# Kernel optimization log

Hardware: AMD Instinct MI355X
Metric: run time of the kernel (lower is better)

## Reference

```python
import jax, jax.numpy as jnp
import numpy as np

D_MODEL = 512
D_INNER = 1024   # expand * d_model
D_STATE = 16
DT_RANK = 32     # ceil(d_model / 16)
D_CONV = 4
BATCH = 4
SEQLEN = 2304
DILATIONS = (1, 2, 4)


def _dw(x, w, pad, dil=1):
    # depthwise 1D conv: x (B,C,L), w (C,1,K)
    return jax.lax.conv_general_dilated(
        x, w, window_strides=(1,), padding=[pad], rhs_dilation=(dil,),
        dimension_numbers=('NCH', 'OIH', 'NCH'), feature_group_count=x.shape[1])


def setup_inputs() -> dict:
    key = jax.random.key(0)
    ks = iter(jax.random.split(key, 32))
    nrm = lambda shape, s=0.02: jax.random.normal(next(ks), shape, jnp.float32) * s
    std = DT_RANK ** -0.5
    return dict(
        hidden_states=jax.random.normal(next(ks), (BATCH, SEQLEN, D_MODEL), jnp.float32),
        in_proj_w=nrm((5 * D_INNER, D_MODEL)),
        conv1d_w=nrm((D_INNER, 1, D_CONV), 0.2),
        conv1d_b=jnp.zeros((D_INNER,), jnp.float32),
        x_proj_w=nrm((DT_RANK + 2 * D_STATE, D_INNER)),
        dt_proj_w=jax.random.uniform(next(ks), (D_INNER, DT_RANK), jnp.float32, -std, std),
        dt_proj_b=jax.random.uniform(next(ks), (D_INNER,), jnp.float32, -5.0, -1.0),
        A_log=jnp.log(jnp.broadcast_to(jnp.arange(1, D_STATE + 1, dtype=jnp.float32), (D_INNER, D_STATE))),
        D=jnp.ones((D_INNER,), jnp.float32),
        out_proj_w=nrm((D_MODEL, 3 * D_INNER)),
        cb_local_w=nrm((D_MODEL, 1, 3), 0.2), cb_local_b=jnp.zeros((D_MODEL,), jnp.float32),
        cb_global_w=nrm((D_MODEL, 1, 1), 0.2), cb_global_b=jnp.zeros((D_MODEL,), jnp.float32),
        cb_pre_w=nrm((3, D_MODEL, 1, 1), 0.2), cb_pre_b=jnp.zeros((3, D_MODEL), jnp.float32),
        cb_dil_w=nrm((3, D_MODEL, 1, 3), 0.2), cb_dil_b=jnp.zeros((3, D_MODEL), jnp.float32),
        cb_ln_g=jnp.ones((4 * D_MODEL,), jnp.float32), cb_ln_b=jnp.zeros((4 * D_MODEL,), jnp.float32),
        cb_fuse_w=nrm((2 * D_MODEL, 4 * D_MODEL, 1)), cb_fuse_b=jnp.zeros((2 * D_MODEL,), jnp.float32),
    )


def reference(hidden_states, in_proj_w, conv1d_w, conv1d_b, x_proj_w, dt_proj_w,
              dt_proj_b, A_log, D, out_proj_w, cb_local_w, cb_local_b,
              cb_global_w, cb_global_b, cb_pre_w, cb_pre_b, cb_dil_w, cb_dil_b,
              cb_ln_g, cb_ln_b, cb_fuse_w, cb_fuse_b):
    B, L, dm = hidden_states.shape
    d_inner = D.shape[0]
    d_state = A_log.shape[1]
    dt_rank = dt_proj_w.shape[1]

    # in_proj -> (B, 5*d_inner, L)
    xz = jnp.einsum('ed,bld->bel', in_proj_w, hidden_states)
    xz_f = xz[:, :2 * d_inner]
    xz_b = xz[:, 2 * d_inner:4 * d_inner]
    xz_1 = xz[:, 4 * d_inner:]
    # bidirectional: stack forward and time-flipped backward along batch
    xzc = jnp.concatenate([xz_f, jnp.flip(xz_b, -1)], axis=0)  # (2B, 2*d_inner, L)
    x, z = xzc[:, :d_inner], xzc[:, d_inner:]

    # causal depthwise conv + SiLU
    kc = conv1d_w.shape[-1]
    x = _dw(x, conv1d_w, (kc - 1, 0)) + conv1d_b[None, :, None]
    x = jax.nn.silu(x)

    # x_proj -> dt, B, C
    x_dbl = jnp.einsum('kd,bdl->bkl', x_proj_w, x)
    dt = x_dbl[:, :dt_rank]
    Bm = x_dbl[:, dt_rank:dt_rank + d_state]
    Cm = x_dbl[:, dt_rank + d_state:]
    delta = jax.nn.softplus(jnp.einsum('dr,brl->bdl', dt_proj_w, dt) + dt_proj_b[None, :, None])
    A = -jnp.exp(A_log)  # (d, n)

    # selective scan over time
    delta_l = jnp.moveaxis(delta, 2, 0)  # (L, 2B, d)
    u_l = jnp.moveaxis(x, 2, 0)          # (L, 2B, d)
    B_l = jnp.moveaxis(Bm, 2, 0)         # (L, 2B, n)
    C_l = jnp.moveaxis(Cm, 2, 0)         # (L, 2B, n)

    def step(h, t):
        dl, ul, Bl, Cl = t
        dA = jnp.exp(dl[..., None] * A)                    # (2B, d, n)
        h = dA * h + (dl * ul)[..., None] * Bl[:, None, :]
        y = jnp.einsum('bdn,bn->bd', h, Cl)
        return h, y

    h0 = jnp.zeros((x.shape[0], d_inner, d_state), x.dtype)
    _, ys = jax.lax.scan(step, h0, (delta_l, u_l, B_l, C_l))
    y = jnp.moveaxis(ys, 0, 2)  # (2B, d, L)
    y = y + D[None, :, None] * x
    y = y * jax.nn.silu(z)
    out = jnp.concatenate([y[:B], jnp.flip(y[B:], -1)], axis=1)  # (B, 2*d_inner, L)

    # ConvBranch on xz_1 (2*dm channels -> split into xa, xc of dm each)
    xa, xc = xz_1[:, :dm], xz_1[:, dm:]
    local = jax.nn.gelu(_dw(xc, cb_local_w, (1, 1)) + cb_local_b[None, :, None], approximate=False)
    phi = jax.nn.relu(cb_global_w[:, 0, 0][None, :] * xc.mean(-1) + cb_global_b[None, :])  # (B, dm)
    feats = []
    for i, d in enumerate(DILATIONS):
        xp = cb_pre_w[i, :, 0, 0][None, :, None] * xa + cb_pre_b[i][None, :, None]
        feats.append(_dw(xp, cb_dil_w[i], (d, d), dil=d) + cb_dil_b[i][None, :, None])
    cat = jnp.concatenate(feats + [phi[:, :, None] * local], axis=1)  # (B, 4*dm, L)
    c = cat.transpose(0, 2, 1)
    mu = c.mean(-1, keepdims=True)
    var = c.var(-1, keepdims=True)
    c = (c - mu) / jnp.sqrt(var + 1e-5) * cb_ln_g + cb_ln_b
    cat = c.transpose(0, 2, 1)
    out_c = jnp.einsum('oc,bcl->bol', cb_fuse_w[:, :, 0], cat) + cb_fuse_b[None, :, None]  # (B, 2*d_inner... = d_inner? no: 2*dm, L)

    out_f = jnp.concatenate([out, out_c], axis=1)  # (B, 3*d_inner, L)
    return jnp.einsum('md,bdl->blm', out_proj_w, out_f)  # (B, L, d_model)
```

## Files before the change

kernel.cpp:

```cpp
#include <hip/hip_runtime.h>
#include <math.h>

#define L 2304
#define NB 4
#define NCH 36
#define STILE 64
#define SPAD 68
#define DLU_PAD 130

typedef __attribute__((ext_vector_type(8))) short short8v;
typedef __attribute__((ext_vector_type(4))) float f32x4;

__device__ inline unsigned short f2bf(float x) {
    unsigned u = __float_as_uint(x);
    return (unsigned short)((u + 0x7fffu + ((u >> 16) & 1u)) >> 16);
}
__device__ inline void split1(float x, unsigned short& h, unsigned short& l) {
    h = f2bf(x);
    float hf = __uint_as_float((unsigned)h << 16);
    l = f2bf(x - hf);
}

__device__ __forceinline__ void gload16(const unsigned short* g, unsigned short* l)
{
    __builtin_amdgcn_global_load_lds(
        (const __attribute__((address_space(1))) unsigned int*)g,
        (__attribute__((address_space(3))) unsigned int*)l, 16, 0, 0);
}

__device__ inline float row_reduce16(float v) {
    v += __int_as_float(__builtin_amdgcn_update_dpp(0, __float_as_int(v), 0xB1, 0xF, 0xF, true));
    v += __int_as_float(__builtin_amdgcn_update_dpp(0, __float_as_int(v), 0x4E, 0xF, 0xF, true));
    v += __int_as_float(__builtin_amdgcn_update_dpp(0, __float_as_int(v), 0x124, 0xF, 0xF, true));
    v += __int_as_float(__builtin_amdgcn_update_dpp(0, __float_as_int(v), 0x128, 0xF, 0xF, true));
    return v;
}

__global__ __launch_bounds__(256) void split_kernel(
    const float* __restrict__ src, unsigned short* __restrict__ hi,
    unsigned short* __restrict__ lo, int n)
{
    int i = (blockIdx.x * 256 + threadIdx.x) * 4;
    if (i >= n) return;
    float4 v = *(const float4*)(src + i);
    unsigned short h0, h1, h2, h3, l0, l1, l2, l3;
    split1(v.x, h0, l0); split1(v.y, h1, l1);
    split1(v.z, h2, l2); split1(v.w, h3, l3);
    ushort4 hv; hv.x = h0; hv.y = h1; hv.z = h2; hv.w = h3;
    ushort4 lv; lv.x = l0; lv.y = l1; lv.z = l2; lv.w = l3;
    *(ushort4*)(hi + i) = hv;
    *(ushort4*)(lo + i) = lv;
}

__global__ __launch_bounds__(256) void split_t_kernel(
    const float* __restrict__ src, unsigned short* __restrict__ hiT,
    unsigned short* __restrict__ loT, int C)
{
    __shared__ float tile[64][65];
    const int l0 = blockIdx.x * 64, c0 = blockIdx.y * 64;
    const int li = threadIdx.x & 63, q = threadIdx.x >> 6;
    for (int cc = q; cc < 64; cc += 4)
        tile[cc][li] = src[(long)(c0 + cc) * L + l0 + li];
    __syncthreads();
    const int ci = threadIdx.x & 63;
    for (int ll = q; ll < 64; ll += 4) {
        float x = tile[ci][ll];
        unsigned short h, l;
        split1(x, h, l);
        long o = (long)(l0 + ll) * C + c0 + ci;
        hiT[o] = h;
        loT[o] = l;
    }
}

__global__ __launch_bounds__(256) void gemm_mfma(
    const unsigned short* __restrict__ Ahi, const unsigned short* __restrict__ Alo, int lda,
    const unsigned short* __restrict__ Bhi, const unsigned short* __restrict__ Blo, int ldb,
    float* __restrict__ C, long cms, long cns, int K, int act,
    const float* __restrict__ emu, const float* __restrict__ ers,
    const float* __restrict__ es1, const float* __restrict__ es2)
{
    __shared__ unsigned short Ah[128 * 32], Al[128 * 32], Bh[128 * 32], Bl[128 * 32];
    const int tid = threadIdx.x;
    const int lane = tid & 63, wave = tid >> 6;
    const int wm = (wave >> 1) * 64, wn = (wave & 1) * 64;
    const int m0 = blockIdx.x * 128, n0 = blockIdx.y * 128;
    const int rowS = tid >> 2;
    const int cS = ((tid & 3) ^ ((tid >> 3) & 3)) * 8;
    const unsigned short* gAh0 = Ahi + (long)(m0 + rowS) * lda + cS;
    const unsigned short* gAl0 = Alo + (long)(m0 + rowS) * lda + cS;
    const unsigned short* gBh0 = Bhi + (long)(n0 + rowS) * ldb + cS;
    const unsigned short* gBl0 = Blo + (long)(n0 + rowS) * ldb + cS;
    const long a64 = (long)64 * lda, b64 = (long)64 * ldb;
    unsigned short* lAh0 = Ah + tid * 8;  unsigned short* lAh1 = Ah + 2048 + tid * 8;
    unsigned short* lAl0 = Al + tid * 8;  unsigned short* lAl1 = Al + 2048 + tid * 8;
    unsigned short* lBh0 = Bh + tid * 8;  unsigned short* lBh1 = Bh + 2048 + tid * 8;
    unsigned short* lBl0 = Bl + tid * 8;  unsigned short* lBl1 = Bl + 2048 + tid * 8;
    const int fr = lane & 15;
    const int chq = (((lane >> 4) ^ ((fr >> 1) & 3)) << 3);

    f32x4 acc[4][4];
#pragma unroll
    for (int i = 0; i < 4; ++i)
#pragma unroll
        for (int j = 0; j < 4; ++j) acc[i][j] = (f32x4){0.f, 0.f, 0.f, 0.f};

    for (int k0 = 0; k0 < K; k0 += 32) {
        gload16(gAh0 + k0, lAh0); gload16(gAh0 + a64 + k0, lAh1);
        gload16(gAl0 + k0, lAl0); gload16(gAl0 + a64 + k0, lAl1);
        gload16(gBh0 + k0, lBh0); gload16(gBh0 + b64 + k0, lBh1);
        gload16(gBl0 + k0, lBl0); gload16(gBl0 + b64 + k0, lBl1);
        __syncthreads();
        short8v bhf[4], blf[4];
#pragma unroll
        for (int nf = 0; nf < 4; ++nf) {
            bhf[nf] = *(const short8v*)&Bh[(wn + nf * 16 + fr) * 32 + chq];
            blf[nf] = *(const short8v*)&Bl[(wn + nf * 16 + fr) * 32 + chq];
        }
#pragma unroll
        for (int mf = 0; mf < 4; ++mf) {
            short8v ah = *(const short8v*)&Ah[(wm + mf * 16 + fr) * 32 + chq];
            short8v al = *(const short8v*)&Al[(wm + mf * 16 + fr) * 32 + chq];
#pragma unroll
            for (int nf = 0; nf < 4; ++nf) {
                acc[mf][nf] = __builtin_amdgcn_mfma_f32_16x16x32_bf16(ah, bhf[nf], acc[mf][nf], 0, 0, 0);
                acc[mf][nf] = __builtin_amdgcn_mfma_f32_16x16x32_bf16(ah, blf[nf], acc[mf][nf], 0, 0, 0);
                acc[mf][nf] = __builtin_amdgcn_mfma_f32_16x16x32_bf16(al, bhf[nf], acc[mf][nf], 0, 0, 0);
            }
        }
        __syncthreads();
    }
    const int rb = (lane >> 4) * 4;
#pragma unroll
    for (int mf = 0; mf < 4; ++mf) {
#pragma unroll
        for (int nf = 0; nf < 4; ++nf) {
            int n = n0 + wn + nf * 16 + fr;
            int mb = m0 + wm + mf * 16 + rb;
            if (cms == 1) {
                float4 r;
                r.x = acc[mf][nf][0]; r.y = acc[mf][nf][1];
                r.z = acc[mf][nf][2]; r.w = acc[mf][nf][3];
                *(float4*)(C + (long)n * cns + mb) = r;
            } else {
#pragma unroll
                for (int r = 0; r < 4; ++r) {
                    int m = mb + r;
                    float v = acc[mf][nf][r];
                    if (act == 2) v = (v - emu[n] * es1[m]) * ers[n] + es2[m];
                    C[(long)m * cms + n] = v;
                }
            }
        }
    }
}

__global__ __launch_bounds__(256) void gemm_mfma128sk(
    const unsigned short* __restrict__ Ahi, const unsigned short* __restrict__ Alo, int lda,
    const unsigned short* __restrict__ Bhi, const unsigned short* __restrict__ Blo, int ldb,
    float* __restrict__ P, int KS, int Mstride)
{
    __shared__ unsigned short Ah[128 * 32], Al[128 * 32], Bh[128 * 32], Bl[128 * 32];
    const int tid = threadIdx.x;
    const int lane = tid & 63, wave = tid >> 6;
    const int wm = (wave >> 1) * 64, wn = (wave & 1) * 64;
    const int nwg = gridDim.x * gridDim.y * gridDim.z;
    const int bid = blockIdx.x + gridDim.x * (blockIdx.y + gridDim.y * blockIdx.z);
    const int cpx = nwg >> 3;
    const int swz = (bid & 7) * cpx + (bid >> 3);
    const int bx = swz % gridDim.x;
    const int rest = swz / gridDim.x;
    const int by = rest % gridDim.y;
    const int sl = rest / gridDim.y;
    const int m0 = bx * 128, n0 = by * 128;
    const int kbase = sl * KS;
    const int rowS = tid >> 2;
    const int cS = ((tid & 3) ^ ((tid >> 3) & 3)) * 8;
    const unsigned short* gAh0 = Ahi + (long)(m0 + rowS) * lda + kbase + cS;
    const unsigned short* gAl0 = Alo + (long)(m0 + rowS) * lda + kbase + cS;
    const unsigned short* gBh0 = Bhi + (long)(n0 + rowS) * ldb + kbase + cS;
    const unsigned short* gBl0 = Blo + (long)(n0 + rowS) * ldb + kbase + cS;
    const long a64 = (long)64 * lda, b64 = (long)64 * ldb;
    unsigned short* lAh0 = Ah + tid * 8;  unsigned short* lAh1 = Ah + 2048 + tid * 8;
    unsigned short* lAl0 = Al + tid * 8;  unsigned short* lAl1 = Al + 2048 + tid * 8;
    unsigned short* lBh0 = Bh + tid * 8;  unsigned short* lBh1 = Bh + 2048 + tid * 8;
    unsigned short* lBl0 = Bl + tid * 8;  unsigned short* lBl1 = Bl + 2048 + tid * 8;
    const int fr = lane & 15;
    const int chq = (((lane >> 4) ^ ((fr >> 1) & 3)) << 3);

    f32x4 acc[4][4];
#pragma unroll
    for (int i = 0; i < 4; ++i)
#pragma unroll
        for (int j = 0; j < 4; ++j) acc[i][j] = (f32x4){0.f, 0.f, 0.f, 0.f};

    for (int k0 = 0; k0 < KS; k0 += 32) {
        gload16(gAh0 + k0, lAh0); gload16(gAh0 + a64 + k0, lAh1);
        gload16(gAl0 + k0, lAl0); gload16(gAl0 + a64 + k0, lAl1);
        gload16(gBh0 + k0, lBh0); gload16(gBh0 + b64 + k0, lBh1);
        gload16(gBl0 + k0, lBl0); gload16(gBl0 + b64 + k0, lBl1);
        __syncthreads();
        short8v bhf[4], blf[4];
#pragma unroll
        for (int nf = 0; nf < 4; ++nf) {
            bhf[nf] = *(const short8v*)&Bh[(wn + nf * 16 + fr) * 32 + chq];
            blf[nf] = *(const short8v*)&Bl[(wn + nf * 16 + fr) * 32 + chq];
        }
#pragma unroll
        for (int mf = 0; mf < 4; ++mf) {
            short8v ah = *(const short8v*)&Ah[(wm + mf * 16 + fr) * 32 + chq];
            short8v al = *(const short8v*)&Al[(wm + mf * 16 + fr) * 32 + chq];
#pragma unroll
            for (int nf = 0; nf < 4; ++nf) {
                acc[mf][nf] = __builtin_amdgcn_mfma_f32_16x16x32_bf16(ah, bhf[nf], acc[mf][nf], 0, 0, 0);
                acc[mf][nf] = __builtin_amdgcn_mfma_f32_16x16x32_bf16(ah, blf[nf], acc[mf][nf], 0, 0, 0);
                acc[mf][nf] = __builtin_amdgcn_mfma_f32_16x16x32_bf16(al, bhf[nf], acc[mf][nf], 0, 0, 0);
            }
        }
        __syncthreads();
    }
    const int rb = (lane >> 4) * 4;
    float* Pp = P + (long)sl * Mstride * L;
#pragma unroll
    for (int mf = 0; mf < 4; ++mf) {
#pragma unroll
        for (int nf = 0; nf < 4; ++nf) {
            int n = n0 + wn + nf * 16 + fr;
            int mb = m0 + wm + mf * 16 + rb;
            float4 r;
            r.x = acc[mf][nf][0]; r.y = acc[mf][nf][1];
            r.z = acc[mf][nf][2]; r.w = acc[mf][nf][3];
            *(float4*)(Pp + (long)n * Mstride + mb) = r;
        }
    }
}

__global__ __launch_bounds__(256) void out_reduce(
    const float* __restrict__ P, float* __restrict__ out)
{
    const long E = (long)512 * L;
    long i = ((long)blockIdx.x * 256 + threadIdx.x) * 4;
    float4 r = *(const float4*)(P + i);
#pragma unroll
    for (int s = 1; s < 8; ++s) {
        float4 a = *(const float4*)(P + (long)s * E + i);
        r.x += a.x; r.y += a.y; r.z += a.z; r.w += a.w;
    }
    *(float4*)(out + i) = r;
}

__global__ __launch_bounds__(256) void fuse_reduce_bt(
    const float* __restrict__ P,
    const float* __restrict__ emu, const float* __restrict__ ers,
    const float* __restrict__ es1, const float* __restrict__ es2,
    unsigned short* __restrict__ BT_hi, unsigned short* __restrict__ BT_lo)
{
    const long E = (long)1024 * L;
    long idx = (long)blockIdx.x * 256 + threadIdx.x;
    int l = (int)(idx >> 8);
    int dq = (int)(idx & 255) * 4;
    long base = (long)l * 1024 + dq;
    float4 a = *(const float4*)(P + base);
    float4 b = *(const float4*)(P + E + base);
    float4 c = *(const float4*)(P + 2 * E + base);
    float4 d = *(const float4*)(P + 3 * E + base);
    float v[4];
    v[0] = (a.x + b.x) + (c.x + d.x);
    v[1] = (a.y + b.y) + (c.y + d.y);
    v[2] = (a.z + b.z) + (c.z + d.z);
    v[3] = (a.w + b.w) + (c.w + d.w);
    float mu = emu[l], rs = ers[l];
    unsigned short hv[4], lv[4];
#pragma unroll
    for (int j = 0; j < 4; ++j) {
        int m = dq + j;
        float x = (v[j] - mu * es1[m]) * rs + es2[m];
        split1(x, hv[j], lv[j]);
    }
    long o = (long)l * 3072 + 2048 + dq;
    ushort4 h4; h4.x = hv[0]; h4.y = hv[1]; h4.z = hv[2]; h4.w = hv[3];
    ushort4 l4; l4.x = lv[0]; l4.y = lv[1]; l4.z = lv[2]; l4.w = lv[3];
    *(ushort4*)(BT_hi + o) = h4;
    *(ushort4*)(BT_lo + o) = l4;
}

__global__ __launch_bounds__(256) void gemm_f32(
    const float* __restrict__ A, int lda,
    const float* __restrict__ B, long ldb, int b_nk, long bbs,
    float* __restrict__ C, long cms, long cns, long cbs,
    int M, int N, int K,
    const float* __restrict__ bias, int act,
    const float* __restrict__ emu, const float* __restrict__ ers,
    const float* __restrict__ es1, const float* __restrict__ es2)
{
    __shared__ float As[16][65];
    __shared__ float Bs[16][65];
    const int tid = threadIdx.x;
    const int tx = tid & 15, ty = tid >> 4;
    const int m0 = blockIdx.x * 64, n0 = blockIdx.y * 64;
    const int bz = blockIdx.z;
    const float* Bb = B + (long)bz * bbs;
    float acc[4][4];
#pragma unroll
    for (int i = 0; i < 4; ++i)
#pragma unroll
        for (int j = 0; j < 4; ++j) acc[i][j] = 0.f;

    for (int k0 = 0; k0 < K; k0 += 16) {
        {
            int m = tid >> 2, kq = (tid & 3) << 2;
            float4 v = *(const float4*)(A + (long)(m0 + m) * lda + (k0 + kq));
            As[kq + 0][m] = v.x; As[kq + 1][m] = v.y; As[kq + 2][m] = v.z; As[kq + 3][m] = v.w;
        }
        if (b_nk) {
            int n = tid >> 2, kq = (tid & 3) << 2;
            float4 v = *(const float4*)(Bb + (long)(n0 + n) * ldb + (k0 + kq));
            Bs[kq + 0][n] = v.x; Bs[kq + 1][n] = v.y; Bs[kq + 2][n] = v.z; Bs[kq + 3][n] = v.w;
        } else {
            int k = tid >> 4, nq = (tid & 15) << 2;
            float4 v = *(const float4*)(Bb + (long)(k0 + k) * ldb + (n0 + nq));
            Bs[k][nq + 0] = v.x; Bs[k][nq + 1] = v.y; Bs[k][nq + 2] = v.z; Bs[k][nq + 3] = v.w;
        }
        __syncthreads();
#pragma unroll
        for (int kk = 0; kk < 16; ++kk) {
            float a[4], b[4];
#pragma unroll
            for (int i = 0; i < 4; ++i) a[i] = As[kk][ty * 4 + i];
#pragma unroll
            for (int j = 0; j < 4; ++j) b[j] = Bs[kk][tx * 4 + j];
#pragma unroll
            for (int i = 0; i < 4; ++i)
#pragma unroll
                for (int j = 0; j < 4; ++j) acc[i][j] = fmaf(a[i], b[j], acc[i][j]);
        }
        __syncthreads();
    }
#pragma unroll
    for (int i = 0; i < 4; ++i) {
        int m = m0 + ty * 4 + i;
        float bs = bias ? bias[m] : 0.f;
        float s1 = es1 ? es1[m] : 0.f;
        float s2 = es2 ? es2[m] : 0.f;
#pragma unroll
        for (int j = 0; j < 4; ++j) {
            int n = n0 + tx * 4 + j;
            float v = acc[i][j] + bs;
            if (act == 1) v = (v > 20.f) ? v : log1pf(expf(v));
            else if (act == 2) {
                float mu = emu[n];
                float rs = ers[n];
                v = (v - mu * s1) * rs + s2;
            }
            C[(long)bz * cbs + (long)m * cms + (long)n * cns] = v;
        }
    }
}

__global__ __launch_bounds__(256) void xproj_partial(
    const float* __restrict__ W, const float* __restrict__ xconv,
    float* __restrict__ P)
{
    __shared__ float As[16][65];
    __shared__ float Bs[16][65];
    const int tid = threadIdx.x;
    const int tx = tid & 15, ty = tid >> 4;
    const int n0 = blockIdx.x * 64;
    const int dir = blockIdx.y, sl = blockIdx.z;
    const float* A = W + sl * 256;
    const float* B = xconv + ((long)dir * 1024 + sl * 256) * L;
    float* Pp = P + ((long)sl * 2 + dir) * 64 * L;
    float acc[4][4];
#pragma unroll
    for (int i = 0; i < 4; ++i)
#pragma unroll
        for (int j = 0; j < 4; ++j) acc[i][j] = 0.f;

    for (int k0 = 0; k0 < 256; k0 += 16) {
        {
            int m = tid >> 2, kq = (tid & 3) << 2;
            float4 v = *(const float4*)(A + (long)m * 1024 + (k0 + kq));
            As[kq + 0][m] = v.x; As[kq + 1][m] = v.y; As[kq + 2][m] = v.z; As[kq + 3][m] = v.w;
        }
        {
            int k = tid >> 4, nq = (tid & 15) << 2;
            float4 v = *(const float4*)(B + (long)(k0 + k) * L + (n0 + nq));
            Bs[k][nq + 0] = v.x; Bs[k][nq + 1] = v.y; Bs[k][nq + 2] = v.z; Bs[k][nq + 3] = v.w;
        }
        __syncthreads();
#pragma unroll
        for (int kk = 0; kk < 16; ++kk) {
            float a[4], b[4];
#pragma unroll
            for (int i = 0; i < 4; ++i) a[i] = As[kk][ty * 4 + i];
#pragma unroll
            for (int j = 0; j < 4; ++j) b[j] = Bs[kk][tx * 4 + j];
#pragma unroll
            for (int i = 0; i < 4; ++i)
#pragma unroll
                for (int j = 0; j < 4; ++j) acc[i][j] = fmaf(a[i], b[j], acc[i][j]);
        }
        __syncthreads();
    }
#pragma unroll
    for (int i = 0; i < 4; ++i) {
        int m = ty * 4 + i;
        float4 r;
        r.x = acc[i][0]; r.y = acc[i][1]; r.z = acc[i][2]; r.w = acc[i][3];
        *(float4*)(Pp + (long)m * L + n0 + tx * 4) = r;
    }
}

__global__ __launch_bounds__(256) void xproj_reduce(
    const float* __restrict__ P, float* __restrict__ xdbl)
{
    const long E = (long)2 * 64 * L;
    long i = ((long)blockIdx.x * 256 + threadIdx.x) * 4;
    float4 a = *(const float4*)(P + i);
    float4 b = *(const float4*)(P + E + i);
    float4 c = *(const float4*)(P + 2 * E + i);
    float4 d = *(const float4*)(P + 3 * E + i);
    float4 r;
    r.x = (a.x + b.x) + (c.x + d.x);
    r.y = (a.y + b.y) + (c.y + d.y);
    r.z = (a.z + b.z) + (c.z + d.z);
    r.w = (a.w + b.w) + (c.w + d.w);
    *(float4*)(xdbl + i) = r;
}

__global__ __launch_bounds__(256) void mamba_conv_kernel(
    const float* __restrict__ xz_b, const float* __restrict__ w,
    const float* __restrict__ bias, float* __restrict__ xout)
{
    long idx = (long)blockIdx.x * 256 + threadIdx.x;
    int l = (int)(idx % L);
    long r = idx / L;
    int d = (int)(r % 1024);
    int dir = (int)(r / 1024);
    const float* src = xz_b + ((dir ? 2048 : 0) + (long)d) * L;
    float acc = bias[d];
#pragma unroll
    for (int j = 0; j < 4; ++j) {
        int t = l - 3 + j;
        if (t >= 0) {
            float v = dir ? src[L - 1 - t] : src[t];
            acc = fmaf(w[d * 4 + j], v, acc);
        }
    }
    xout[idx] = acc / (1.f + expf(-acc));
}

__global__ __launch_bounds__(256) void scan_pass1(
    const float* __restrict__ delta_b, const float* __restrict__ xconv_b,
    const float* __restrict__ xdbl_b, const float* __restrict__ A_log,
    float* __restrict__ hend, float* __restrict__ pAb)
{
    __shared__ float s_dlu[16][DLU_PAD];
    __shared__ float s_B[16][SPAD];
    const int tid = threadIdx.x;
    const int dir = blockIdx.y, ch = blockIdx.z;
    const int n = tid & 15, dloc = tid >> 4;
    const int d0 = blockIdx.x * 16;
    const int d = d0 + dloc;
    const int t0 = ch * STILE;
    const float Adn = -expf(A_log[d * 16 + n]);
    const float* dl_p = delta_b + ((long)dir * 1024 + d0) * L;
    const float* u_p  = xconv_b + ((long)dir * 1024 + d0) * L;
    const float* B_p  = xdbl_b + ((long)dir * 64 + 32) * L;
    const int lch = tid >> 4, lq = tid & 15;
    {
        float4 a = *(const float4*)(dl_p + (long)lch * L + t0 + lq * 4);
        float4 b = *(const float4*)(u_p + (long)lch * L + t0 + lq * 4);
        float4 w0; w0.x = a.x; w0.y = b.x; w0.z = a.y; w0.w = b.y;
        float4 w1; w1.x = a.z; w1.y = b.z; w1.z = a.w; w1.w = b.w;
        *(float4*)&s_dlu[lch][lq * 8] = w0;
        *(float4*)&s_dlu[lch][lq * 8 + 4] = w1;
        float4 v = *(const float4*)(B_p + (long)lch * L + t0 + lq * 4);
        *(float4*)&s_B[lch][lq * 4] = v;
    }
    __syncthreads();
    float h = 0.f, p = 1.f;
#pragma unroll 4
    for (int tt = 0; tt < STILE; ++tt) {
        float2 dlu = *(const float2*)&s_dlu[dloc][tt * 2];
        float Bv = s_B[n][tt];
        float dA = __expf(dlu.x * Adn);
        h = fmaf(dA, h, dlu.x * dlu.y * Bv);
        p *= dA;
    }
    long sidx = (((long)dir * NCH + ch) * 1024 + d) * 16 + n;
    hend[sidx] = h;
    pAb[sidx] = p;
}

__global__ __launch_bounds__(256) void scan_fix(
    const float* __restrict__ hend, const float* __restrict__ pAb,
    float* __restrict__ hin)
{
    int tid = blockIdx.x * 256 + threadIdx.x;
    int dir = tid >> 14;
    int rest = tid & 16383;
    float h = 0.f;
#pragma unroll
    for (int c = 0; c < NCH; ++c) {
        long idx = (((long)dir * NCH + c) << 14) + rest;
        hin[idx] = h;
        h = hend[idx] + pAb[idx] * h;
    }
}

__global__ __launch_bounds__(256) void scan_pass2_bt(
    const float* __restrict__ delta_b, const float* __restrict__ xconv_b,
    const float* __restrict__ xdbl_b, const float* __restrict__ xz_b,
    const float* __restrict__ A_log, const float* __restrict__ Dvec,
    const float* __restrict__ hin,
    unsigned short* __restrict__ BT_hi, unsigned short* __restrict__ BT_lo)
{
    __shared__ float s_dlu[16][DLU_PAD];
    __shared__ float s_BC[16][DLU_PAD];
    const int tid = threadIdx.x;
    const int dir = blockIdx.y, ch = blockIdx.z;
    const int n = tid & 15, dloc = tid >> 4;
    const int d0 = blockIdx.x * 16;
    const int d = d0 + dloc;
    const int t0 = ch * STILE;
    const int opos0 = dir ? (L - STILE - t0) : t0;
    const float Adn = -expf(A_log[d * 16 + n]);
    const float Dd = Dvec[d];
    const float* dl_p = delta_b + ((long)dir * 1024 + d0) * L;
    const float* u_p  = xconv_b + ((long)dir * 1024 + d0) * L;
    const float* B_p  = xdbl_b + ((long)dir * 64 + 32) * L;
    const float* C_p  = xdbl_b + ((long)dir * 64 + 48) * L;
    const float* z_base = xz_b + ((dir ? 3072 : 1024) + (long)d0) * L;
    const int lch = tid >> 4, lq = tid & 15;
    {
        float4 a = *(const float4*)(dl_p + (long)lch * L + t0 + lq * 4);
        float4 b = *(const float4*)(u_p + (long)lch * L + t0 + lq * 4);
        float4 w0; w0.x = a.x; w0.y = b.x; w0.z = a.y; w0.w = b.y;
        float4 w1; w1.x = a.z; w1.y = b.z; w1.z = a.w; w1.w = b.w;
        *(float4*)&s_dlu[lch][lq * 8] = w0;
        *(float4*)&s_dlu[lch][lq * 8 + 4] = w1;
        float4 c = *(const float4*)(B_p + (long)lch * L + t0 + lq * 4);
        float4 e = *(const float4*)(C_p + (long)lch * L + t0 + lq * 4);
        float4 x0; x0.x = c.x; x0.y = e.x; x0.z = c.y; x0.w = e.y;
        float4 x1; x1.x = c.z; x1.y = e.z; x1.z = c.w; x1.w = e.w;
        *(float4*)&s_BC[lch][lq * 8] = x0;
        *(float4*)&s_BC[lch][lq * 8 + 4] = x1;
    }
    __syncthreads();
    float h = hin[(((long)dir * NCH + ch) * 1024 + d) * 16 + n];
#pragma unroll 4
    for (int tt = 0; tt < STILE; ++tt) {
        float2 dlu = *(const float2*)&s_dlu[dloc][tt * 2];
        float2 bc = *(const float2*)&s_BC[n][tt * 2];
        float dA = __expf(dlu.x * Adn);
        h = fmaf(dA, h, dlu.x * dlu.y * bc.x);
        float y = row_reduce16(h * bc.y);
        if (n == 0) s_dlu[dloc][tt * 2] = y + Dd * dlu.y;
    }
    __syncthreads();
    {
        const int p = tid >> 2;
        const int dq = (tid & 3) * 4;
        const int l = opos0 + p;
        const int cbase = (dir ? 1024 : 0) + d0;
        const int yi = (dir ? 63 - p : p) * 2;
        unsigned short hv[4], lv[4];
#pragma unroll
        for (int j = 0; j < 4; ++j) {
            int dl = dq + j;
            float y = s_dlu[dl][yi];
            float z = z_base[(long)dl * L + l];
            float v = y * (z / (1.f + __expf(-z)));
            split1(v, hv[j], lv[j]);
        }
        long o = (long)l * 3072 + cbase + dq;
        ushort4 h4; h4.x = hv[0]; h4.y = hv[1]; h4.z = hv[2]; h4.w = hv[3];
        ushort4 l4; l4.x = lv[0]; l4.y = lv[1]; l4.z = lv[2]; l4.w = lv[3];
        *(ushort4*)(BT_hi + o) = h4;
        *(ushort4*)(BT_lo + o) = l4;
    }
}

__global__ __launch_bounds__(256) void scan_pass2(
    const float* __restrict__ delta_b, const float* __restrict__ xconv_b,
    const float* __restrict__ xdbl_b, const float* __restrict__ xz_b,
    const float* __restrict__ A_log, const float* __restrict__ Dvec,
    const float* __restrict__ hin, float* __restrict__ out_fb)
{
    __shared__ float s_dlu[16][DLU_PAD];
    __shared__ float s_BC[16][DLU_PAD];
    const int tid = threadIdx.x;
    const int dir = blockIdx.y, ch = blockIdx.z;
    const int n = tid & 15, dloc = tid >> 4;
    const int d0 = blockIdx.x * 16;
    const int d = d0 + dloc;
    const int t0 = ch * STILE;
    const int opos0 = dir ? (L - STILE - t0) : t0;
    const float Adn = -expf(A_log[d * 16 + n]);
    const float Dd = Dvec[d];
    const float* dl_p = delta_b + ((long)dir * 1024 + d0) * L;
    const float* u_p  = xconv_b + ((long)dir * 1024 + d0) * L;
    const float* B_p  = xdbl_b + ((long)dir * 64 + 32) * L;
    const float* C_p  = xdbl_b + ((long)dir * 64 + 48) * L;
    const float* z_p  = xz_b + ((dir ? 3072 : 1024) + (long)d0) * L;
    float* o_p = out_fb + ((dir ? 1024 : 0) + (long)d0) * L;
    const int lch = tid >> 4, lq = tid & 15;
    {
        float4 a = *(const float4*)(dl_p + (long)lch * L + t0 + lq * 4);
        float4 b = *(const float4*)(u_p + (long)lch * L + t0 + lq * 4);
        float4 w0; w0.x = a.x; w0.y = b.x; w0.z = a.y; w0.w = b.y;
        float4 w1; w1.x = a.z; w1.y = b.z; w1.z = a.w; w1.w = b.w;
        *(float4*)&s_dlu[lch][lq * 8] = w0;
        *(float4*)&s_dlu[lch][lq * 8 + 4] = w1;
        float4 c = *(const float4*)(B_p + (long)lch * L + t0 + lq * 4);
        float4 e = *(const float4*)(C_p + (long)lch * L + t0 + lq * 4);
        float4 x0; x0.x = c.x; x0.y = e.x; x0.z = c.y; x0.w = e.y;
        float4 x1; x1.x = c.z; x1.y = e.z; x1.z = c.w; x1.w = e.w;
        *(float4*)&s_BC[lch][lq * 8] = x0;
        *(float4*)&s_BC[lch][lq * 8 + 4] = x1;
    }
    __syncthreads();
    float h = hin[(((long)dir * NCH + ch) * 1024 + d) * 16 + n];
#pragma unroll 4
    for (int tt = 0; tt < STILE; ++tt) {
        float2 dlu = *(const float2*)&s_dlu[dloc][tt * 2];
        float2 bc = *(const float2*)&s_BC[n][tt * 2];
        float dA = __expf(dlu.x * Adn);
        h = fmaf(dA, h, dlu.x * dlu.y * bc.x);
        float y = row_reduce16(h * bc.y);
        if (n == 0) s_dlu[dloc][tt * 2] = y + Dd * dlu.y;
    }
    {
        float* po = o_p + (long)lch * L + opos0;
        const float* pz = z_p + (long)lch * L + opos0;
        int oo = lq * 4;
        float4 zv = *(const float4*)(pz + oo);
        float y0 = s_dlu[lch][(dir ? 63 - oo : oo) * 2];
        float y1 = s_dlu[lch][(dir ? 62 - oo : oo + 1) * 2];
        float y2 = s_dlu[lch][(dir ? 61 - oo : oo + 2) * 2];
        float y3 = s_dlu[lch][(dir ? 60 - oo : oo + 3) * 2];
        float4 r;
        r.x = y0 * (zv.x / (1.f + __expf(-zv.x)));
        r.y = y1 * (zv.y / (1.f + __expf(-zv.y)));
        r.z = y2 * (zv.z / (1.f + __expf(-zv.z)));
        r.w = y3 * (zv.w / (1.f + __expf(-zv.w)));
        *(float4*)(po + oo) = r;
    }
}

__global__ __launch_bounds__(256) void mean_phi_kernel(
    const float* __restrict__ xz_b, const float* __restrict__ gw,
    const float* __restrict__ gb, float* __restrict__ phi_b)
{
    int c = blockIdx.x;
    const float* src = xz_b + (4608 + (long)c) * L;
    float s = 0.f;
    for (int l = threadIdx.x; l < L; l += 256) s += src[l];
    __shared__ float red[256];
    red[threadIdx.x] = s;
    __syncthreads();
    for (int st = 128; st > 0; st >>= 1) {
        if (threadIdx.x < st) red[threadIdx.x] += red[threadIdx.x + st];
        __syncthreads();
    }
    if (threadIdx.x == 0) {
        float m = red[0] / (float)L;
        phi_b[c] = fmaxf(gw[c] * m + gb[c], 0.f);
    }
}

__global__ __launch_bounds__(256) void cat_build_kernel(
    const float* __restrict__ xz_b,
    const float* __restrict__ lw, const float* __restrict__ lb,
    const float* __restrict__ pw, const float* __restrict__ pb,
    const float* __restrict__ dw, const float* __restrict__ db,
    const float* __restrict__ phi_b, float* __restrict__ cat_b)
{
    long idx = (long)blockIdx.x * 256 + threadIdx.x;
    int l = (int)(idx % L);
    int cc = (int)(idx / L);
    float val;
    if (cc < 1536) {
        int i = cc >> 9, c = cc & 511, dil = 1 << i;
        const float* xa = xz_b + (4096 + (long)c) * L;
        float pwv = pw[i * 512 + c], pbv = pb[i * 512 + c];
        const float* w = dw + ((long)i * 512 + c) * 3;
        float acc = db[i * 512 + c];
#pragma unroll
        for (int k = 0; k < 3; ++k) {
            int t = l + (k - 1) * dil;
            if (t >= 0 && t < L) acc += (pwv * xa[t] + pbv) * w[k];
        }
        val = acc;
    } else {
        int c = cc & 511;
        const float* xc = xz_b + (4608 + (long)c) * L;
        float acc = lb[c];
#pragma unroll
        for (int k = 0; k < 3; ++k) {
            int t = l - 1 + k;
            if (t >= 0 && t < L) acc += xc[t] * lw[c * 3 + k];
        }
        float g = 0.5f * acc * (1.f + erff(acc * 0.70710678118f));
        val = phi_b[c] * g;
    }
    cat_b[idx] = val;
}

__global__ __launch_bounds__(256) void ln_partial_kernel(
    const float* __restrict__ cat_b, float* __restrict__ ps, float* __restrict__ pq)
{
    int l = blockIdx.x * 256 + threadIdx.x;
    int g = blockIdx.y;
    const float* p = cat_b + (long)g * 64 * L + l;
    float s = 0.f, q = 0.f;
#pragma unroll 8
    for (int c = 0; c < 64; ++c) {
        float v = p[(long)c * L];
        s += v;
        q = fmaf(v, v, q);
    }
    ps[g * L + l] = s;
    pq[g * L + l] = q;
}

__global__ __launch_bounds__(256) void ln_final_kernel(
    const float* __restrict__ ps, const float* __restrict__ pq,
    float* __restrict__ mu_b, float* __restrict__ rsig_b)
{
    int l = blockIdx.x * 256 + threadIdx.x;
    float s = 0.f, q = 0.f;
#pragma unroll
    for (int g = 0; g < 32; ++g) {
        s += ps[g * L + l];
        q += pq[g * L + l];
    }
    float m = s * (1.f / 2048.f);
    float var = q * (1.f / 2048.f) - m * m;
    mu_b[l] = m;
    rsig_b[l] = rsqrtf(var + 1e-5f);
}

__global__ __launch_bounds__(256) void ln_stats_kernel(
    const float* __restrict__ cat_b, float* __restrict__ mu_b, float* __restrict__ rsig_b)
{
    int tx = threadIdx.x & 63, ty = threadIdx.x >> 6;
    int l = blockIdx.x * 64 + tx;
    float s = 0.f, s2 = 0.f;
    for (int c = ty; c < 2048; c += 4) {
        float v = cat_b[(long)c * L + l];
        s += v;
        s2 += v * v;
    }
    __shared__ float rs[4][64], rq[4][64];
    rs[ty][tx] = s;
    rq[ty][tx] = s2;
    __syncthreads();
    if (ty == 0) {
        float S = rs[0][tx] + rs[1][tx] + rs[2][tx] + rs[3][tx];
        float Q = rq[0][tx] + rq[1][tx] + rq[2][tx] + rq[3][tx];
        float m = S * (1.f / 2048.f);
        float var = Q * (1.f / 2048.f) - m * m;
        mu_b[l] = m;
        rsig_b[l] = rsqrtf(var + 1e-5f);
    }
}

__global__ __launch_bounds__(256) void fuse_pre_kernel(
    const float* __restrict__ fw, const float* __restrict__ g,
    const float* __restrict__ lbn, const float* __restrict__ fb,
    float* __restrict__ wg, float* __restrict__ S1, float* __restrict__ S2)
{
    int o = blockIdx.x;
    float s1 = 0.f, s2 = 0.f;
    for (int c = threadIdx.x; c < 2048; c += 256) {
        float w = fw[(long)o * 2048 + c];
        float v = w * g[c];
        wg[(long)o * 2048 + c] = v;
        s1 += v;
        s2 += w * lbn[c];
    }
    __shared__ float r1[256], r2[256];
    r1[threadIdx.x] = s1;
    r2[threadIdx.x] = s2;
    __syncthreads();
    for (int st = 128; st > 0; st >>= 1) {
        if (threadIdx.x < st) {
            r1[threadIdx.x] += r1[threadIdx.x + st];
            r2[threadIdx.x] += r2[threadIdx.x + st];
        }
        __syncthreads();
    }
    if (threadIdx.x == 0) {
        S1[o] = r1[0];
        S2[o] = r2[0] + fb[o];
    }
}

__global__ __launch_bounds__(256) void fuse_pre_split_kernel(
    const float* __restrict__ fw, const float* __restrict__ g,
    const float* __restrict__ lbn, const float* __restrict__ fb,
    unsigned short* __restrict__ wg_hi, unsigned short* __restrict__ wg_lo,
    float* __restrict__ S1, float* __restrict__ S2)
{
    int o = blockIdx.x;
    float s1 = 0.f, s2 = 0.f;
    for (int c = threadIdx.x; c < 2048; c += 256) {
        float w = fw[(long)o * 2048 + c];
        float v = w * g[c];
        unsigned short h, l;
        split1(v, h, l);
        wg_hi[(long)o * 2048 + c] = h;
        wg_lo[(long)o * 2048 + c] = l;
        s1 += v;
        s2 += w * lbn[c];
    }
    __shared__ float r1[256], r2[256];
    r1[threadIdx.x] = s1;
    r2[threadIdx.x] = s2;
    __syncthreads();
    for (int st = 128; st > 0; st >>= 1) {
        if (threadIdx.x < st) {
            r1[threadIdx.x] += r1[threadIdx.x + st];
            r2[threadIdx.x] += r2[threadIdx.x + st];
        }
        __syncthreads();
    }
    if (threadIdx.x == 0) {
        S1[o] = r1[0];
        S2[o] = r2[0] + fb[o];
    }
}

extern "C" void kernel_launch(void* const* d_in, const int* in_sizes, int n_in,
                              void* d_out, int out_size, void* d_ws, size_t ws_size,
                              hipStream_t stream)
{
    const float* hidden     = (const float*)d_in[0];
    const float* in_proj_w  = (const float*)d_in[1];
    const float* conv1d_w   = (const float*)d_in[2];
    const float* conv1d_b   = (const float*)d_in[3];
    const float* x_proj_w   = (const float*)d_in[4];
    const float* dt_proj_w  = (const float*)d_in[5];
    const float* dt_proj_b  = (const float*)d_in[6];
    const float* A_log      = (const float*)d_in[7];
    const float* Dvec       = (const float*)d_in[8];
    const float* out_proj_w = (const float*)d_in[9];
    const float* cb_local_w = (const float*)d_in[10];
    const float* cb_local_b = (const float*)d_in[11];
    const float* cb_global_w= (const float*)d_in[12];
    const float* cb_global_b= (const float*)d_in[13];
    const float* cb_pre_w   = (const float*)d_in[14];
    const float* cb_pre_b   = (const float*)d_in[15];
    const float* cb_dil_w   = (const float*)d_in[16];
    const float* cb_dil_b   = (const float*)d_in[17];
    const float* cb_ln_g    = (const float*)d_in[18];
    const float* cb_ln_b    = (const float*)d_in[19];
    const float* cb_fuse_w  = (const float*)d_in[20];
    const float* cb_fuse_b  = (const float*)d_in[21];

    float* ws = (float*)d_ws;
    const size_t CSZ = (size_t)2 * NCH * 1024 * 16;

    size_t off = 0;
    float* S1    = ws + off; off += 1024;
    float* S2    = ws + off; off += 1024;
    float* xz_b  = ws + off; off += (size_t)5120 * L;
    float* out_fb= ws + off; off += (size_t)3072 * L;
    float* cat_b = ws + off; off += (size_t)2048 * L;
    float* delta_b = cat_b;
    float* xconv_b = ws + off; off += (size_t)2048 * L;
    float* xdbl_b  = ws + off; off += (size_t)128 * L;
    float* mu_b    = ws + off; off += L;
    float* rsig_b  = ws + off; off += L;
    float* phi_b   = ws + off; off += 512;
    float* lnps    = ws + off; off += (size_t)32 * L;
    float* lnpq    = ws + off; off += (size_t)32 * L;
    float* hend = ws + off; off += CSZ;
    float* pAb  = ws + off; off += CSZ;
    float* hin  = ws + off; off += CSZ;
    unsigned short* wg_hi  = (unsigned short*)(ws + off); off += (size_t)1024 * 2048 / 2;
    unsigned short* wg_lo  = (unsigned short*)(ws + off); off += (size_t)1024 * 2048 / 2;
    unsigned short* inW_hi = (unsigned short*)(ws + off); off += (size_t)5120 * 512 / 2;
    unsigned short* inW_lo = (unsigned short*)(ws + off); off += (size_t)5120 * 512 / 2;
    unsigned short* outW_hi= (unsigned short*)(ws + off); off += (size_t)512 * 3072 / 2;
    unsigned short* outW_lo= (unsigned short*)(ws + off); off += (size_t)512 * 3072 / 2;
    unsigned short* BT_hi  = (unsigned short*)(ws + off); off += (size_t)3072 * L / 2;
    unsigned short* BT_lo  = (unsigned short*)(ws + off); off += (size_t)3072 * L / 2;
    size_t need_mfma = off * sizeof(float);

    float* xpP = out_fb;
    float* fsP = cat_b;
    float* opP = cat_b;

    if (ws_size >= need_mfma) {
        fuse_pre_split_kernel<<<1024, 256, 0, stream>>>(
            cb_fuse_w, cb_ln_g, cb_ln_b, cb_fuse_b, wg_hi, wg_lo, S1, S2);
        split_kernel<<<(5120 * 512) / 1024, 256, 0, stream>>>(in_proj_w, inW_hi, inW_lo, 5120 * 512);
        split_kernel<<<(512 * 3072) / 1024, 256, 0, stream>>>(out_proj_w, outW_hi, outW_lo, 512 * 3072);

        for (int b = 0; b < NB; ++b) {
            const float* hid_b = hidden + (size_t)b * L * 512;
            float* out_b = (float*)d_out + (size_t)b * L * 512;

            split_kernel<<<(L * 512) / 1024, 256, 0, stream>>>(hid_b, BT_hi, BT_lo, L * 512);
            gemm_mfma<<<dim3(5120 / 128, L / 128), 256, 0, stream>>>(
                inW_hi, inW_lo, 512, BT_hi, BT_lo, 512,
                xz_b, L, 1, 512, 0, nullptr, nullptr, nullptr, nullptr);

            mean_phi_kernel<<<512, 256, 0, stream>>>(xz_b, cb_global_w, cb_global_b, phi_b);
            cat_build_kernel<<<(2048 * L) / 256, 256, 0, stream>>>(
                xz_b, cb_local_w, cb_local_b, cb_pre_w, cb_pre_b, cb_dil_w, cb_dil_b, phi_b, cat_b);
            ln_partial_kernel<<<dim3(L / 256, 32), 256, 0, stream>>>(cat_b, lnps, lnpq);
            ln_final_kernel<<<L / 256, 256, 0, stream>>>(lnps, lnpq, mu_b, rsig_b);
            split_t_kernel<<<dim3(L / 64, 2048 / 64), 256, 0, stream>>>(cat_b, BT_hi, BT_lo, 2048);
            gemm_mfma128sk<<<dim3(1024 / 128, L / 128, 4), 256, 0, stream>>>(
                wg_hi, wg_lo, 2048, BT_hi, BT_lo, 2048, fsP, 512, 1024);
            fuse_reduce_bt<<<L, 256, 0, stream>>>(
                fsP, mu_b, rsig_b, S1, S2, BT_hi, BT_lo);

            mamba_conv_kernel<<<(2 * 1024 * L) / 256, 256, 0, stream>>>(
                xz_b, conv1d_w, conv1d_b, xconv_b);
            xproj_partial<<<dim3(L / 64, 2, 4), 256, 0, stream>>>(
                x_proj_w, xconv_b, xpP);
            xproj_reduce<<<(2 * 64 * L / 4) / 256, 256, 0, stream>>>(xpP, xdbl_b);
            gemm_f32<<<dim3(1024 / 64, L / 64, 2), 256, 0, stream>>>(
                dt_proj_w, 32, xdbl_b, L, 0, (long)64 * L,
                delta_b, L, 1, (long)1024 * L, 1024, L, 32,
                dt_proj_b, 1, nullptr, nullptr, nullptr, nullptr);
            scan_pass1<<<dim3(64, 2, NCH), 256, 0, stream>>>(
                delta_b, xconv_b, xdbl_b, A_log, hend, pAb);
            scan_fix<<<128, 256, 0, stream>>>(hend, pAb, hin);
            scan_pass2_bt<<<dim3(64, 2, NCH), 256, 0, stream>>>(
                delta_b, xconv_b, xdbl_b, xz_b, A_log, Dvec, hin, BT_hi, BT_lo);

            gemm_mfma128sk<<<dim3(512 / 128, L / 128, 8), 256, 0, stream>>>(
                outW_hi, outW_lo, 3072, BT_hi, BT_lo, 3072, opP, 384, 512);
            out_reduce<<<(512 * L / 4) / 256, 256, 0, stream>>>(opP, out_b);
        }
        return;
    }

    off = 0;
    float* wg    = ws + off; off += (size_t)1024 * 2048;
    S1    = ws + off; off += 1024;
    S2    = ws + off; off += 1024;
    xz_b  = ws + off; off += (size_t)5120 * L;
    out_fb= ws + off; off += (size_t)3072 * L;
    cat_b = ws + off; off += (size_t)2048 * L;
    delta_b = cat_b;
    xconv_b = ws + off; off += (size_t)2048 * L;
    xdbl_b  = ws + off; off += (size_t)128 * L;
    mu_b    = ws + off; off += L;
    rsig_b  = ws + off; off += L;
    phi_b   = ws + off; off += 512;
    hend = ws + off; off += CSZ;
    pAb  = ws + off; off += CSZ;
    hin  = ws + off; off += CSZ;
    if (ws_size < off * sizeof(float)) return;

    fuse_pre_kernel<<<1024, 256, 0, stream>>>(cb_fuse_w, cb_ln_g, cb_ln_b, cb_fuse_b, wg, S1, S2);

    for (int b = 0; b < NB; ++b) {
        const float* hid_b = hidden + (size_t)b * L * 512;
        float* out_b = (float*)d_out + (size_t)b * L * 512;

        gemm_f32<<<dim3(5120 / 64, L / 64, 1), 256, 0, stream>>>(
            in_proj_w, 512, hid_b, 512, 1, 0,
            xz_b, L, 1, 0, 5120, L, 512,
            nullptr, 0, nullptr, nullptr, nullptr, nullptr);

        mean_phi_kernel<<<512, 256, 0, stream>>>(xz_b, cb_global_w, cb_global_b, phi_b);
        cat_build_kernel<<<(2048 * L) / 256, 256, 0, stream>>>(
            xz_b, cb_local_w, cb_local_b, cb_pre_w, cb_pre_b, cb_dil_w, cb_dil_b, phi_b, cat_b);
        ln_stats_kernel<<<L / 64, 256, 0, stream>>>(cat_b, mu_b, rsig_b);
        gemm_f32<<<dim3(1024 / 64, L / 64, 1), 256, 0, stream>>>(
            wg, 2048, cat_b, L, 0, 0,
            out_fb + (long)2048 * L, L, 1, 0, 1024, L, 2048,
            nullptr, 2, mu_b, rsig_b, S1, S2);

        mamba_conv_kernel<<<(2 * 1024 * L) / 256, 256, 0, stream>>>(
            xz_b, conv1d_w, conv1d_b, xconv_b);
        gemm_f32<<<dim3(1, L / 64, 2), 256, 0, stream>>>(
            x_proj_w, 1024, xconv_b, L, 0, (long)1024 * L,
            xdbl_b, L, 1, (long)64 * L, 64, L, 1024,
            nullptr, 0, nullptr, nullptr, nullptr, nullptr);
        gemm_f32<<<dim3(1024 / 64, L / 64, 2), 256, 0, stream>>>(
            dt_proj_w, 32, xdbl_b, L, 0, (long)64 * L,
            delta_b, L, 1, (long)1024 * L, 1024, L, 32,
            dt_proj_b, 1, nullptr, nullptr, nullptr, nullptr);
        scan_pass1<<<dim3(64, 2, NCH), 256, 0, stream>>>(
            delta_b, xconv_b, xdbl_b, A_log, hend, pAb);
        scan_fix<<<128, 256, 0, stream>>>(hend, pAb, hin);
        scan_pass2<<<dim3(64, 2, NCH), 256, 0, stream>>>(
            delta_b, xconv_b, xdbl_b, xz_b, A_log, Dvec, hin, out_fb);

        gemm_f32<<<dim3(512 / 64, L / 64, 1), 256, 0, stream>>>(
            out_proj_w, 3072, out_fb, L, 0, 0,
            out_b, 1, 512, 0, 512, L, 3072,
            nullptr, 0, nullptr, nullptr, nullptr, nullptr);
    }
}
```

Measured before the change: 1.237 ms.

## Fuse dt_proj GEMM and softplus into both selective-scan passes

Drops the separate gemm_f32 that wrote the delta tensor (2x1024xL floats per batch) and instead computes delta = softplus(dt_proj_w · dt + b) inside scan_pass1f and scan_pass2f_bt from the 32-row dt slice of xdbl staged in shared memory. This removes a global write and two global reads of delta per batch, plus one kernel launch. In exchange the small 32-deep dot product and softplus are computed twice, once in each scan pass, and both kernels use more shared memory, which may lower occupancy.

```diff
diff --git a/kernel.cpp b/kernel.cpp
--- a/kernel.cpp
+++ b/kernel.cpp
@@ -450,6 +450,74 @@
     xout[idx] = acc / (1.f + expf(-acc));
 }
 
+__global__ __launch_bounds__(256) void scan_pass1f(
+    const float* __restrict__ xconv_b, const float* __restrict__ xdbl_b,
+    const float* __restrict__ A_log,
+    const float* __restrict__ dtw, const float* __restrict__ dtb,
+    float* __restrict__ hend, float* __restrict__ pAb)
+{
+    __shared__ float s_dlu[16][DLU_PAD];
+    __shared__ float s_B[16][SPAD];
+    __shared__ float s_dt[32][68];
+    __shared__ float s_w[16][33];
+    const int tid = threadIdx.x;
+    const int dir = blockIdx.y, ch = blockIdx.z;
+    const int n = tid & 15, dloc = tid >> 4;
+    const int d0 = blockIdx.x * 16;
+    const int d = d0 + dloc;
+    const int t0 = ch * STILE;
+    const float Adn = -expf(A_log[d * 16 + n]);
+    const float* u_p  = xconv_b + ((long)dir * 1024 + d0) * L;
+    const float* B_p  = xdbl_b + ((long)dir * 64 + 32) * L;
+    const float* dt_p = xdbl_b + ((long)dir * 64) * L;
+    const int lch = tid >> 4, lq = tid & 15;
+    {
+        float4 b = *(const float4*)(u_p + (long)lch * L + t0 + lq * 4);
+        s_dlu[lch][(lq * 4 + 0) * 2 + 1] = b.x;
+        s_dlu[lch][(lq * 4 + 1) * 2 + 1] = b.y;
+        s_dlu[lch][(lq * 4 + 2) * 2 + 1] = b.z;
+        s_dlu[lch][(lq * 4 + 3) * 2 + 1] = b.w;
+        float4 v = *(const float4*)(B_p + (long)lch * L + t0 + lq * 4);
+        *(float4*)&s_B[lch][lq * 4] = v;
+        int kk = tid >> 3, cc = (tid & 7) * 8;
+        float4 t0v = *(const float4*)(dt_p + (long)kk * L + t0 + cc);
+        float4 t1v = *(const float4*)(dt_p + (long)kk * L + t0 + cc + 4);
+        *(float4*)&s_dt[kk][cc] = t0v;
+        *(float4*)&s_dt[kk][cc + 4] = t1v;
+        float2 wv = *(const float2*)(dtw + (long)(d0 + lch) * 32 + lq * 2);
+        s_w[lch][lq * 2] = wv.x;
+        s_w[lch][lq * 2 + 1] = wv.y;
+    }
+    __syncthreads();
+    {
+        float bias = dtb[d0 + lch];
+#pragma unroll
+        for (int j = 0; j < 4; ++j) {
+            int l = lq * 4 + j;
+            float acc = 0.f;
+#pragma unroll
+            for (int k = 0; k < 32; ++k)
+                acc = fmaf(s_w[lch][k], s_dt[k][l], acc);
+            float v = acc + bias;
+            v = (v > 20.f) ? v : log1pf(expf(v));
+            s_dlu[lch][l * 2] = v;
+        }
+    }
+    __syncthreads();
+    float h = 0.f, p = 1.f;
+#pragma unroll 4
+    for (int tt = 0; tt < STILE; ++tt) {
+        float2 dlu = *(const float2*)&s_dlu[dloc][tt * 2];
+        float Bv = s_B[n][tt];
+        float dA = __expf(dlu.x * Adn);
+        h = fmaf(dA, h, dlu.x * dlu.y * Bv);
+        p *= dA;
+    }
+    long sidx = (((long)dir * NCH + ch) * 1024 + d) * 16 + n;
+    hend[sidx] = h;
+    pAb[sidx] = p;
+}
+
 __global__ __launch_bounds__(256) void scan_pass1(
     const float* __restrict__ delta_b, const float* __restrict__ xconv_b,
     const float* __restrict__ xdbl_b, const float* __restrict__ A_log,
@@ -509,15 +577,18 @@
     }
 }
 
-__global__ __launch_bounds__(256) void scan_pass2_bt(
-    const float* __restrict__ delta_b, const float* __restrict__ xconv_b,
-    const float* __restrict__ xdbl_b, const float* __restrict__ xz_b,
+__global__ __launch_bounds__(256) void scan_pass2f_bt(
+    const float* __restrict__ xconv_b, const float* __restrict__ xdbl_b,
+    const float* __restrict__ xz_b,
     const float* __restrict__ A_log, const float* __restrict__ Dvec,
+    const float* __restrict__ dtw, const float* __restrict__ dtb,
     const float* __restrict__ hin,
     unsigned short* __restrict__ BT_hi, unsigned short* __restrict__ BT_lo)
 {
     __shared__ float s_dlu[16][DLU_PAD];
     __shared__ float s_BC[16][DLU_PAD];
+    __shared__ float s_dt[32][68];
+    __shared__ float s_w[16][33];
     const int tid = threadIdx.x;
     const int dir = blockIdx.y, ch = blockIdx.z;
     const int n = tid & 15, dloc = tid >> 4;
@@ -527,25 +598,47 @@
     const int opos0 = dir ? (L - STILE - t0) : t0;
     const float Adn = -expf(A_log[d * 16 + n]);
     const float Dd = Dvec[d];
-    const float* dl_p = delta_b + ((long)dir * 1024 + d0) * L;
     const float* u_p  = xconv_b + ((long)dir * 1024 + d0) * L;
     const float* B_p  = xdbl_b + ((long)dir * 64 + 32) * L;
     const float* C_p  = xdbl_b + ((long)dir * 64 + 48) * L;
+    const float* dt_p = xdbl_b + ((long)dir * 64) * L;
     const float* z_base = xz_b + ((dir ? 3072 : 1024) + (long)d0) * L;
     const int lch = tid >> 4, lq = tid & 15;
     {
-        float4 a = *(const float4*)(dl_p + (long)lch * L + t0 + lq * 4);
         float4 b = *(const float4*)(u_p + (long)lch * L + t0 + lq * 4);
-        float4 w0; w0.x = a.x; w0.y = b.x; w0.z = a.y; w0.w = b.y;
-        float4 w1; w1.x = a.z; w1.y = b.z; w1.z = a.w; w1.w = b.w;
-        *(float4*)&s_dlu[lch][lq * 8] = w0;
-        *(float4*)&s_dlu[lch][lq * 8 + 4] = w1;
+        s_dlu[lch][(lq * 4 + 0) * 2 + 1] = b.x;
+        s_dlu[lch][(lq * 4 + 1) * 2 + 1] = b.y;
+        s_dlu[lch][(lq * 4 + 2) * 2 + 1] = b.z;
+        s_dlu[lch][(lq * 4 + 3) * 2 + 1] = b.w;
         float4 c = *(const float4*)(B_p + (long)lch * L + t0 + lq * 4);
         float4 e = *(const float4*)(C_p + (long)lch * L + t0 + lq * 4);
         float4 x0; x0.x = c.x; x0.y = e.x; x0.z = c.y; x0.w = e.y;
         float4 x1; x1.x = c.z; x1.y = e.z; x1.z = c.w; x1.w = e.w;
         *(float4*)&s_BC[lch][lq * 8] = x0;
         *(float4*)&s_BC[lch][lq * 8 + 4] = x1;
+        int kk = tid >> 3, cc = (tid & 7) * 8;
+        float4 t0v = *(const float4*)(dt_p + (long)kk * L + t0 + cc);
+        float4 t1v = *(const float4*)(dt_p + (long)kk * L + t0 + cc + 4);
+        *(float4*)&s_dt[kk][cc] = t0v;
+        *(float4*)&s_dt[kk][cc + 4] = t1v;
+        float2 wv = *(const float2*)(dtw + (long)(d0 + lch) * 32 + lq * 2);
+        s_w[lch][lq * 2] = wv.x;
+        s_w[lch][lq * 2 + 1] = wv.y;
+    }
+    __syncthreads();
+    {
+        float bias = dtb[d0 + lch];
+#pragma unroll
+        for (int j = 0; j < 4; ++j) {
+            int l = lq * 4 + j;
+            float acc = 0.f;
+#pragma unroll
+            for (int k = 0; k < 32; ++k)
+                acc = fmaf(s_w[lch][k], s_dt[k][l], acc);
+            float v = acc + bias;
+            v = (v > 20.f) ? v : log1pf(expf(v));
+            s_dlu[lch][l * 2] = v;
+        }
     }
     __syncthreads();
     float h = hin[(((long)dir * NCH + ch) * 1024 + d) * 16 + n];
@@ -869,7 +962,6 @@
     float* xz_b  = ws + off; off += (size_t)5120 * L;
     float* out_fb= ws + off; off += (size_t)3072 * L;
     float* cat_b = ws + off; off += (size_t)2048 * L;
-    float* delta_b = cat_b;
     float* xconv_b = ws + off; off += (size_t)2048 * L;
     float* xdbl_b  = ws + off; off += (size_t)128 * L;
     float* mu_b    = ws + off; off += L;
@@ -925,15 +1017,12 @@
             xproj_partial<<<dim3(L / 64, 2, 4), 256, 0, stream>>>(
                 x_proj_w, xconv_b, xpP);
             xproj_reduce<<<(2 * 64 * L / 4) / 256, 256, 0, stream>>>(xpP, xdbl_b);
-            gemm_f32<<<dim3(1024 / 64, L / 64, 2), 256, 0, stream>>>(
-                dt_proj_w, 32, xdbl_b, L, 0, (long)64 * L,
-                delta_b, L, 1, (long)1024 * L, 1024, L, 32,
-                dt_proj_b, 1, nullptr, nullptr, nullptr, nullptr);
-            scan_pass1<<<dim3(64, 2, NCH), 256, 0, stream>>>(
-                delta_b, xconv_b, xdbl_b, A_log, hend, pAb);
+            scan_pass1f<<<dim3(64, 2, NCH), 256, 0, stream>>>(
+                xconv_b, xdbl_b, A_log, dt_proj_w, dt_proj_b, hend, pAb);
             scan_fix<<<128, 256, 0, stream>>>(hend, pAb, hin);
-            scan_pass2_bt<<<dim3(64, 2, NCH), 256, 0, stream>>>(
-                delta_b, xconv_b, xdbl_b, xz_b, A_log, Dvec, hin, BT_hi, BT_lo);
+            scan_pass2f_bt<<<dim3(64, 2, NCH), 256, 0, stream>>>(
+                xconv_b, xdbl_b, xz_b, A_log, Dvec, dt_proj_w, dt_proj_b,
+                hin, BT_hi, BT_lo);
 
             gemm_mfma128sk<<<dim3(512 / 128, L / 128, 8), 256, 0, stream>>>(
                 outW_hi, outW_lo, 3072, BT_hi, BT_lo, 3072, opP, 384, 512);
@@ -949,7 +1038,7 @@
     xz_b  = ws + off; off += (size_t)5120 * L;
     out_fb= ws + off; off += (size_t)3072 * L;
     cat_b = ws + off; off += (size_t)2048 * L;
-    delta_b = cat_b;
+    float* delta_b = cat_b;
     xconv_b = ws + off; off += (size_t)2048 * L;
     xdbl_b  = ws + off; off += (size_t)128 * L;
     mu_b    = ws + off; off += L;
```

New measurement: 1.301 ms. +5.2%, slower.
